# Kernel optimization log

Hardware: AMD Instinct MI355X
Metric: run time of the kernel (lower is better)

## Reference

```python
import jax, jax.numpy as jnp
import numpy as np
from jax.scipy.optimize import minimize

LAMDA = 0.01        # lamda default in MI()
N_DOMAINS = 2       # domain_label is binary (source/target)
MAXITER = 50        # BFGS iteration budget (torchmin l-bfgs analogue)


def _sq_dists(A, B):
    # squared euclidean pairwise distances == torch.cdist(A, B, p=2) ** 2
    an = jnp.sum(A * A, axis=-1)
    bn = jnp.sum(B * B, axis=-1)
    return an[:, None] + bn[None, :] - 2.0 * (A @ B.T)


def _median_sigma(sf):
    # sigma = median of nonzero squared pairwise source distances.
    # With continuous features the only zeros are the diagonal, so mask it.
    pd = jnp.maximum(_sq_dists(sf, sf), 0.0)
    pd = jnp.where(jnp.eye(pd.shape[0], dtype=bool), jnp.nan, pd)
    return jnp.nanmedian(pd)


def _build(sf, tf, y, l):
    # Gaussian kernel masked by class agreement, plus domain one-hots.
    sigma = _median_sigma(sf)
    X = jnp.concatenate([sf, tf], axis=0)              # [N, d]
    D = _sq_dists(X, X)                                 # [N, N]
    Deltay = (y[:, None] == y[None, :]).astype(X.dtype)
    K_W = jnp.exp(-D / sigma) * Deltay                  # [N, N]
    onehot = jax.nn.one_hot(l[:, 0], N_DOMAINS, dtype=X.dtype)  # [N, 2]
    KD = K_W * (onehot @ onehot.T)                      # K_W * Deltal
    w = jnp.sum(onehot, axis=0) / X.shape[0]            # domain counts / N
    return K_W, KD, onehot, w


def _div(theta, K_W, KD, onehot, w):
    # mean((K_W*Deltal) @ theta) - mean(exp((theta*K_W) @ Deltal - 1))
    # Deltal = onehot @ onehot.T (rank-2), so the second NxN @ NxN matmul
    # collapses to A = K_W @ (theta[:,None]*onehot) with column weights w.
    term1 = jnp.mean(KD @ theta)
    A = K_W @ (theta[:, None] * onehot)                 # [N, 2]
    term2 = jnp.mean(jnp.exp(A - 1.0) @ w)
    return term1 - term2


def _solve_theta(K_W, KD, onehot, w):
    N = K_W.shape[0]
    obj = lambda th: -_div(th, K_W, KD, onehot, w) + LAMDA * (th @ th)
    res = minimize(obj, jnp.zeros((N,), K_W.dtype), method="BFGS",
                   options={"maxiter": MAXITER})
    return res.x


def setup_inputs() -> dict:
    key = jax.random.key(0)
    k1, k2, k3, k4 = jax.random.split(key, 4)
    B, d, n_class = 2048, 256, 31
    source_features = jax.random.normal(k1, (B, d), dtype=jnp.float32)
    target_features = jax.random.normal(k2, (B, d), dtype=jnp.float32)
    y = jax.random.randint(k3, (2 * B,), 0, n_class, dtype=jnp.int32)
    l = jax.random.randint(k4, (2 * B, 1), 0, N_DOMAINS, dtype=jnp.int32)
    return {"source_features": source_features, "target_features": target_features,
            "y": y, "l": l}


def reference(source_features, target_features, y, l):
    K_W, KD, onehot, w = _build(source_features, target_features, y, l)
    theta_hat = _solve_theta(K_W, KD, onehot, w)
    return _div(theta_hat, K_W, KD, onehot, w)
```

## Files before the change

### kernel.cpp

```cpp
#include <hip/hip_runtime.h>
#include <math.h>

#define N_TOT   4096
#define N_SRC   2048
#define DIMF    256
#define NCLASS  31
#define LAMBDA  0.01f

#define K_TRI1  1048063LL
#define K_TRI2  1048064LL

#define WS_ACC    0
#define WS_HIST0  64
#define WS_HISTA  16448
#define WS_HISTB  32832
#define WS_H2A    49216
#define WS_H2B    50240
#define WS_STATE  51264
#define WS_TICK   51520
#define WS_META   52288
#define WS_SCAL   52800
#define ZERO_BYTES 53248
#define WS_PERM   53248
#define WS_XN     69632
#define WS_DS     1048576
#define WS_KBLK   17825792

#define MAXW 224
#define MAXM 112
#define WPAD 116

__device__ __forceinline__ float bf2f(unsigned short h) {
  return __uint_as_float(((unsigned)h) << 16);
}

__device__ __forceinline__ float wredF(float v) {
#pragma unroll
  for (int o = 1; o < 64; o <<= 1) v += __shfl_xor(v, o, 64);
  return v;
}

__device__ __forceinline__ double blockReduceSum(double v, double* red) {
#pragma unroll
  for (int o = 32; o > 0; o >>= 1) v += __shfl_down(v, o, 64);
  int w = threadIdx.x >> 6, lane = threadIdx.x & 63;
  __syncthreads();
  if (lane == 0) red[w] = v;
  __syncthreads();
  return red[0] + red[1] + red[2] + red[3];
}

__device__ __forceinline__ void blockReduceSumMax(double s, double mx, double* red,
                                                  double& os, double& om) {
#pragma unroll
  for (int o = 32; o > 0; o >>= 1) {
    s += __shfl_down(s, o, 64);
    double u = __shfl_down(mx, o, 64);
    mx = fmax(mx, u);
  }
  int w = threadIdx.x >> 6, lane = threadIdx.x & 63;
  __syncthreads();
  if (lane == 0) { red[w] = s; red[4 + w] = mx; }
  __syncthreads();
  os = red[0] + red[1] + red[2] + red[3];
  om = fmax(fmax(red[4], red[5]), fmax(red[6], red[7]));
}

__device__ void scan_find(const unsigned* hist, int nbins, long long k, unsigned* shOut, int tid) {
  __shared__ long long tsum[256];
  int per = nbins / 256;
  long long s = 0;
  for (int q = 0; q < per; q++) s += hist[tid * per + q];
  tsum[tid] = s;
  __syncthreads();
  long long acc = s;
  for (int off = 1; off < 256; off <<= 1) {
    long long add = (tid >= off) ? tsum[tid - off] : 0;
    __syncthreads();
    acc += add;
    tsum[tid] = acc;
    __syncthreads();
  }
  long long run = acc - s;
  for (int q = 0; q < per; q++) {
    unsigned c = hist[tid * per + q];
    if (k >= run && k < run + (long long)c) { shOut[0] = (unsigned)(tid * per + q); shOut[1] = (unsigned)(k - run); }
    run += c;
  }
  __syncthreads();
}

__global__ __launch_bounds__(256) void xn_kernel(const float* __restrict__ sf,
                                                 const float* __restrict__ tf,
                                                 float* __restrict__ xn,
                                                 uint4* __restrict__ wsz,
                                                 const int* __restrict__ y,
                                                 const int* __restrict__ l,
                                                 int* __restrict__ perm,
                                                 int* __restrict__ meta,
                                                 float* __restrict__ scal) {
  __shared__ unsigned cl[64];
  __shared__ unsigned bs2[64];
  __shared__ unsigned cur[64];
  const int tid = threadIdx.x;
  if (blockIdx.x == 0) {
    uint4 z; z.x = 0; z.y = 0; z.z = 0; z.w = 0;
    for (int q = tid; q < ZERO_BYTES / 16; q += 256) wsz[q] = z;
    if (tid < 64) cl[tid] = 0;
    __syncthreads();
    for (int i = tid; i < N_TOT; i += 256) atomicAdd(&cl[y[i] * 2 + l[i]], 1u);
    __syncthreads();
    if (tid == 0) {
      unsigned run = 0;
      for (int b2 = 0; b2 < 62; b2++) { bs2[b2] = run; run += cl[b2]; }
      unsigned run2 = 0, cnt0 = 0;
      for (int c = 0; c < NCLASS; c++) {
        int n = (int)(cl[2 * c] + cl[2 * c + 1]);
        meta[c] = n; meta[32 + c] = (int)cl[2 * c]; meta[64 + c] = (int)bs2[2 * c];
        meta[96 + c] = (int)run2; run2 += (unsigned)(n * n);
        cnt0 += cl[2 * c];
      }
      scal[1] = (float)((double)cnt0 / (4096.0 * 4096.0));
      scal[2] = (float)((double)(N_TOT - cnt0) / (4096.0 * 4096.0));
    }
    __syncthreads();
    if (tid < 64) cur[tid] = bs2[tid];
    __syncthreads();
    for (int i = tid; i < N_TOT; i += 256) {
      int b2 = y[i] * 2 + l[i];
      unsigned pos = atomicAdd(&cur[b2], 1u);
      perm[pos] = i;
    }
  }
  int wid = tid >> 6, lane = tid & 63;
  int row = blockIdx.x * 4 + wid;
  const float* src = (row < N_SRC) ? (sf + (size_t)row * DIMF) : (tf + (size_t)(row - N_SRC) * DIMF);
  float4 v = ((const float4*)src)[lane];
  float s = v.x * v.x + v.y * v.y + v.z * v.z + v.w * v.w;
#pragma unroll
  for (int o = 32; o > 0; o >>= 1) s += __shfl_down(s, o, 64);
  if (lane == 0) xn[row] = s;
}

__global__ __launch_bounds__(256) void dist_k(const float* __restrict__ sf,
                                              const float* __restrict__ xn,
                                              float* __restrict__ Ds,
                                              unsigned* __restrict__ h) {
  __shared__ float As[16][68];
  __shared__ float Bs[16][68];
  __shared__ unsigned lh[2][4096];
  const int tx = threadIdx.x, ty = threadIdx.y;
  const int tid = ty * 16 + tx;
  const int par = tid & 1;
  for (int q = tid; q < 8192; q += 256) lh[q >> 12][q & 4095] = 0;
  int b = blockIdx.x;
  int by = (int)((sqrtf(8.f * (float)b + 1.f) - 1.f) * 0.5f);
  while ((by + 1) * (by + 2) / 2 <= b) ++by;
  while (by * (by + 1) / 2 > b) --by;
  int bx = b - by * (by + 1) / 2;
  const int R = by * 64, C = bx * 64;
  const int si = tid >> 2, sq = tid & 3;
  float4 va = ((const float4*)(sf + (size_t)(R + si) * 256 + 0))[sq];
  float4 vb = ((const float4*)(sf + (size_t)(C + si) * 256 + 0))[sq];
  float acc[4][4] = {};
  for (int kc = 0; kc < 256; kc += 16) {
    As[sq * 4 + 0][si] = va.x; As[sq * 4 + 1][si] = va.y; As[sq * 4 + 2][si] = va.z; As[sq * 4 + 3][si] = va.w;
    Bs[sq * 4 + 0][si] = vb.x; Bs[sq * 4 + 1][si] = vb.y; Bs[sq * 4 + 2][si] = vb.z; Bs[sq * 4 + 3][si] = vb.w;
    __syncthreads();
    if (kc + 16 < 256) {
      va = ((const float4*)(sf + (size_t)(R + si) * 256 + kc + 16))[sq];
      vb = ((const float4*)(sf + (size_t)(C + si) * 256 + kc + 16))[sq];
    }
#pragma unroll
    for (int k = 0; k < 16; k++) {
      float4 a = *(const float4*)&As[k][ty * 4];
      float4 b2 = *(const float4*)&Bs[k][tx * 4];
      acc[0][0] += a.x * b2.x; acc[0][1] += a.x * b2.y; acc[0][2] += a.x * b2.z; acc[0][3] += a.x * b2.w;
      acc[1][0] += a.y * b2.x; acc[1][1] += a.y * b2.y; acc[1][2] += a.y * b2.z; acc[1][3] += a.y * b2.w;
      acc[2][0] += a.z * b2.x; acc[2][1] += a.z * b2.y; acc[2][2] += a.z * b2.z; acc[2][3] += a.z * b2.w;
      acc[3][0] += a.w * b2.x; acc[3][1] += a.w * b2.y; acc[3][2] += a.w * b2.z; acc[3][3] += a.w * b2.w;
    }
    __syncthreads();
  }
  int jbase = C + tx * 4;
  float xnj0 = xn[jbase + 0], xnj1 = xn[jbase + 1], xnj2 = xn[jbase + 2], xnj3 = xn[jbase + 3];
#pragma unroll
  for (int r = 0; r < 4; r++) {
    int i = R + ty * 4 + r;
    float xni = xn[i];
    float v[4];
    v[0] = fmaxf(xni + xnj0 - 2.f * acc[r][0], 0.f);
    v[1] = fmaxf(xni + xnj1 - 2.f * acc[r][1], 0.f);
    v[2] = fmaxf(xni + xnj2 - 2.f * acc[r][2], 0.f);
    v[3] = fmaxf(xni + xnj3 - 2.f * acc[r][3], 0.f);
    if (jbase + 3 < i) {
      float4 o; o.x = v[0]; o.y = v[1]; o.z = v[2]; o.w = v[3];
      ((float4*)&Ds[(size_t)i * 2048 + jbase])[0] = o;
      atomicAdd(&lh[par][__float_as_uint(v[0]) >> 20], 1u);
      atomicAdd(&lh[par][__float_as_uint(v[1]) >> 20], 1u);
      atomicAdd(&lh[par][__float_as_uint(v[2]) >> 20], 1u);
      atomicAdd(&lh[par][__float_as_uint(v[3]) >> 20], 1u);
    } else {
#pragma unroll
      for (int k = 0; k < 4; k++) {
        if (jbase + k < i) {
          Ds[(size_t)i * 2048 + jbase + k] = v[k];
          atomicAdd(&lh[par][__float_as_uint(v[k]) >> 20], 1u);
        }
      }
    }
  }
  __syncthreads();
  for (int q = tid; q < 4096; q += 256) {
    unsigned v = lh[0][q] + lh[1][q];
    if (v) atomicAdd(&h[q], v);
  }
}

__global__ __launch_bounds__(256) void scan0_k(const unsigned* __restrict__ h, unsigned* __restrict__ st) {
  __shared__ unsigned r0[2];
  __shared__ unsigned r1[2];
  scan_find(h, 4096, K_TRI1, r0, threadIdx.x);
  scan_find(h, 4096, K_TRI2, r1, threadIdx.x);
  if (threadIdx.x == 0) { st[0] = r0[0]; st[1] = r0[1]; st[2] = r1[0]; st[3] = r1[1]; }
}

__global__ __launch_bounds__(256) void hist1_k(const float* __restrict__ Ds, const unsigned* __restrict__ st,
                                               unsigned* __restrict__ hA, unsigned* __restrict__ hB) {
  __shared__ unsigned lA[4096];
  __shared__ unsigned lB[4096];
  for (int i = threadIdx.x; i < 4096; i += 256) { lA[i] = 0; lB[i] = 0; }
  __syncthreads();
  unsigned s0 = st[0], s1 = st[2];
  int gw = (blockIdx.x * 256 + threadIdx.x) >> 6;
  int lane = threadIdx.x & 63;
  const float* row = Ds + (size_t)gw * 2048;
  for (int j = lane; j < gw; j += 64) {
    unsigned u = __float_as_uint(row[j]);
    unsigned hi = u >> 20, mid = (u >> 8) & 0xFFFu;
    if (hi == s0) atomicAdd(&lA[mid], 1u);
    if (hi == s1) atomicAdd(&lB[mid], 1u);
  }
  __syncthreads();
  for (int i = threadIdx.x; i < 4096; i += 256) {
    if (lA[i]) atomicAdd(&hA[i], lA[i]);
    if (lB[i]) atomicAdd(&hB[i], lB[i]);
  }
}

__global__ __launch_bounds__(256) void scan1_k(const unsigned* __restrict__ hA, const unsigned* __restrict__ hB,
                                               unsigned* __restrict__ st) {
  __shared__ unsigned r0[2];
  __shared__ unsigned r1[2];
  long long kA = (long long)st[1];
  long long kB = (long long)st[3];
  scan_find(hA, 4096, kA, r0, threadIdx.x);
  scan_find(hB, 4096, kB, r1, threadIdx.x);
  if (threadIdx.x == 0) { st[4] = r0[0]; st[5] = r0[1]; st[6] = r1[0]; st[7] = r1[1]; }
}

__global__ __launch_bounds__(256) void hist2_k(const float* __restrict__ Ds, const unsigned* __restrict__ st,
                                               unsigned* __restrict__ hA, unsigned* __restrict__ hB) {
  __shared__ unsigned lA[256];
  __shared__ unsigned lB[256];
  lA[threadIdx.x] = 0; lB[threadIdx.x] = 0;
  __syncthreads();
  unsigned p0 = (st[0] << 12) | st[4];
  unsigned p1 = (st[2] << 12) | st[6];
  int gw = (blockIdx.x * 256 + threadIdx.x) >> 6;
  int lane = threadIdx.x & 63;
  const float* row = Ds + (size_t)gw * 2048;
  for (int j = lane; j < gw; j += 64) {
    unsigned u = __float_as_uint(row[j]);
    unsigned pre = u >> 8;
    if (pre == p0) atomicAdd(&lA[u & 0xFFu], 1u);
    if (pre == p1) atomicAdd(&lB[u & 0xFFu], 1u);
  }
  __syncthreads();
  if (lA[threadIdx.x]) atomicAdd(&hA[threadIdx.x], lA[threadIdx.x]);
  if (lB[threadIdx.x]) atomicAdd(&hB[threadIdx.x], lB[threadIdx.x]);
}

__global__ __launch_bounds__(256) void scan2b_k(const unsigned* __restrict__ hA, const unsigned* __restrict__ hB,
                                                const unsigned* __restrict__ st, float* __restrict__ scal) {
  int tid = threadIdx.x;
  __shared__ unsigned r0[2];
  __shared__ unsigned r1[2];
  scan_find(hA, 256, (long long)st[5], r0, tid);
  scan_find(hB, 256, (long long)st[7], r1, tid);
  if (tid == 0) {
    unsigned v1 = (st[0] << 20) | (st[4] << 8) | r0[0];
    unsigned v2 = (st[2] << 20) | (st[6] << 8) | r1[0];
    scal[0] = 0.5f * (__uint_as_float(v1) + __uint_as_float(v2));
  }
}

__global__ __launch_bounds__(256) void build_k(const float* __restrict__ sf, const float* __restrict__ tf,
                                               const float* __restrict__ xn, const int* __restrict__ perm,
                                               const int* __restrict__ meta, const float* __restrict__ scal,
                                               float* __restrict__ gK) {
  const int c = blockIdx.z;
  const int n = meta[c];
  const int cs = meta[64 + c];
  const int bo = meta[96 + c];
  const int T = (n + 15) >> 4;
  int b = blockIdx.x;
  if (b >= T * (T + 1) / 2) return;
  int by = (int)((sqrtf(8.f * (float)b + 1.f) - 1.f) * 0.5f);
  while ((by + 1) * (by + 2) / 2 <= b) ++by;
  while (by * (by + 1) / 2 > b) --by;
  int bx = b - by * (by + 1) / 2;
  const int i0 = by * 16, j0 = bx * 16;
  const int tx = threadIdx.x, ty = threadIdx.y;
  __shared__ float As[16][260];
  __shared__ float Bs[16][260];
  __shared__ float ot[16][17];
  __shared__ int ra[16];
  __shared__ int rb[16];
  int tid = ty * 16 + tx;
  if (tid < 16) { int il = i0 + tid; ra[tid] = (il < n) ? perm[cs + il] : -1; }
  else if (tid < 32) { int jl = j0 + tid - 16; rb[tid - 16] = (jl < n) ? perm[cs + jl] : -1; }
  __syncthreads();
  for (int e = tid; e < 1024; e += 256) {
    int r = e >> 6, q = e & 63;
    int g = ra[r];
    if (g >= 0) {
      const float* src = (g < N_SRC) ? (sf + (size_t)g * DIMF) : (tf + (size_t)(g - N_SRC) * DIMF);
      ((float4*)&As[r][q * 4])[0] = ((const float4*)src)[q];
    }
    int g2 = rb[r];
    if (g2 >= 0) {
      const float* src = (g2 < N_SRC) ? (sf + (size_t)g2 * DIMF) : (tf + (size_t)(g2 - N_SRC) * DIMF);
      ((float4*)&Bs[r][q * 4])[0] = ((const float4*)src)[q];
    }
  }
  __syncthreads();
  int il = i0 + ty, jl = j0 + tx;
  float val = 0.f;
  if (il < n && jl < n) {
    float dot = 0.f;
    const float4* a4 = (const float4*)&As[ty][0];
    const float4* b4 = (const float4*)&Bs[tx][0];
#pragma unroll 16
    for (int q = 0; q < 64; q++) {
      float4 a = a4[q], b2 = b4[q];
      dot += a.x * b2.x + a.y * b2.y + a.z * b2.z + a.w * b2.w;
    }
    int gi = ra[ty], gj = rb[tx];
    float d = xn[gi] + xn[gj] - 2.f * dot;
    val = expf(-d / scal[0]);
    gK[(size_t)bo + (size_t)il * n + jl] = val;
  }
  ot[ty][tx] = val;
  __syncthreads();
  if (by != bx) {
    int il2 = j0 + ty, jl2 = i0 + tx;
    if (il2 < n && jl2 < n) gK[(size_t)bo + (size_t)il2 * n + jl2] = ot[tx][ty];
  }
}

__global__ __launch_bounds__(256) void solver_k(const float* __restrict__ gK, const int* __restrict__ meta,
                                                const float* __restrict__ scal, double* __restrict__ acc,
                                                unsigned* __restrict__ tick, float* __restrict__ out) {
  const int c = blockIdx.x >> 1, d = blockIdx.x & 1;
  const int n = meta[c];
  const int m0 = meta[32 + c];
  const int m = d ? (n - m0) : m0;
  const int c0 = d ? m0 : 0;
  const int bo = meta[96 + c];
  const float gamma = scal[1 + d];
  const int tid = threadIdx.x;
  const int wv = tid >> 6, lane = tid & 63;

  __shared__ unsigned short Wl[MAXW * WPAD];
  __shared__ float pS[4 * MAXM];
  __shared__ float pD[4 * MAXM];
  __shared__ float Av[MAXW];
  __shared__ float Sv[MAXW];
  __shared__ float Uv[MAXW];
  __shared__ float bc[MAXM];
  __shared__ float gv[MAXM];
  __shared__ float dgv[MAXM];
  __shared__ alignas(16) float th[128];
  __shared__ alignas(16) float pv[128];
  __shared__ alignas(16) float xv[128];
  __shared__ double red[16];
  __shared__ double gds[2];
  __shared__ float alf_s[2];
  __shared__ int cgst[2];

  const float* K = gK + bo;
  const int st = n;
  const int mp2 = (m + 1) & ~1;
  const int mp4 = (m + 3) & ~3;
  const int iw0 = (n * wv) >> 2, iw1 = (n * (wv + 1)) >> 2;
  const int rq = tid >> 2, ql = tid & 3;

  for (int i = rq; i < n; i += 64) {
    const float* Kr = K + (size_t)i * st + c0;
    unsigned short* Wr = Wl + i * WPAD;
    for (int j = ql; j < m; j += 4) {
      unsigned u = __float_as_uint(Kr[j]);
      u += 0x7fffu + ((u >> 16) & 1u);
      Wr[j] = (unsigned short)(u >> 16);
    }
    if (ql == 0) for (int j = m; j < mp4; j++) Wr[j] = 0;
  }
  for (int j = rq; j < m; j += 64) {
    const float* Kr = K + (size_t)(c0 + j) * st + c0;
    float s = 0.f;
    for (int r = ql; r < m; r += 4) s += Kr[r];
    s += __shfl_xor(s, 1, 64);
    s += __shfl_xor(s, 2, 64);
    if (ql == 0) bc[j] = s * (1.0f / 4096.0f);
  }
  __syncthreads();
  for (int j = tid; j < 128; j += 256) { th[j] = 0.f; pv[j] = 0.f; xv[j] = 0.f; }
  __syncthreads();

  float av_r = 0.f;

  for (int it = 0; it < 25; it++) {
    double o = 0.0;
    if (it == 0) {
      const float s0c = gamma * expf(-1.f);
      av_r = 0.f;
      for (int i = tid; i < n; i += 256) { Sv[i] = s0c; o += (double)s0c; }
    } else {
      for (int i = tid; i < n; i += 256) {
        const unsigned short* Wr = Wl + i * WPAD;
        float a = 0.f;
#pragma unroll 4
        for (int j = 0; j < mp4; j += 4) {
          unsigned long long u = *(const unsigned long long*)(Wr + j);
          float4 t4 = *(const float4*)(th + j);
          unsigned lo = (unsigned)u, hi = (unsigned)(u >> 32);
          a += __uint_as_float(lo << 16) * t4.x
             + __uint_as_float(lo & 0xffff0000u) * t4.y
             + __uint_as_float(hi << 16) * t4.z
             + __uint_as_float(hi & 0xffff0000u) * t4.w;
        }
        av_r = a;
        float si = gamma * expf(fminf(a - 1.f, 30.f));
        Sv[i] = si; o += (double)si;
      }
      for (int j = tid; j < m; j += 256) {
        float t_ = th[j];
        o += (double)(-bc[j] * t_ + LAMBDA * t_ * t_);
      }
    }
    __syncthreads();
    if (it == 0) {
      for (int j = lane; j < m; j += 64) {
        const unsigned short* Wc = Wl + j;
        float s_ = 0.f, ds_ = 0.f;
        int i = iw0;
        for (; i + 3 < iw1; i += 4) {
          float w0 = bf2f(Wc[(i + 0) * WPAD]), w1 = bf2f(Wc[(i + 1) * WPAD]);
          float w2 = bf2f(Wc[(i + 2) * WPAD]), w3 = bf2f(Wc[(i + 3) * WPAD]);
          float a0 = w0 * Sv[i], a1 = w1 * Sv[i + 1], a2 = w2 * Sv[i + 2], a3 = w3 * Sv[i + 3];
          s_ += a0 + a1 + a2 + a3;
          ds_ += a0 * w0 + a1 * w1 + a2 * w2 + a3 * w3;
        }
        for (; i < iw1; i++) { float w = bf2f(Wc[i * WPAD]); float a = w * Sv[i]; s_ += a; ds_ += a * w; }
        pS[wv * MAXM + j] = s_; pD[wv * MAXM + j] = ds_;
      }
    } else {
      for (int j = lane; j < m; j += 64) {
        const unsigned short* Wc = Wl + j;
        float s_ = 0.f;
        int i = iw0;
        for (; i + 3 < iw1; i += 4)
          s_ += bf2f(Wc[(i+0)*WPAD]) * Sv[i]   + bf2f(Wc[(i+1)*WPAD]) * Sv[i+1]
              + bf2f(Wc[(i+2)*WPAD]) * Sv[i+2] + bf2f(Wc[(i+3)*WPAD]) * Sv[i+3];
        for (; i < iw1; i++) s_ += bf2f(Wc[i * WPAD]) * Sv[i];
        pS[wv * MAXM + j] = s_;
      }
    }
    __syncthreads();
    double gm = 0.0;
    for (int j = tid; j < m; j += 256) {
      float s_ = pS[j] + pS[MAXM + j] + pS[2 * MAXM + j] + pS[3 * MAXM + j];
      if (it == 0) {
        float ds_ = pD[j] + pD[MAXM + j] + pD[2 * MAXM + j] + pD[3 * MAXM + j];
        dgv[j] = ds_ + 2.f * LAMBDA;
      }
      float g = s_ - bc[j] + 2.f * LAMBDA * th[j];
      gv[j] = g;
      double ag = fabs((double)g); if (ag > gm) gm = ag;
    }
    double obj, gmax;
    blockReduceSumMax(o, gm, red, obj, gmax);
    if (gmax < 1e-5) break;

    const float tolf = (it == 0) ? 1e-2f : ((it == 1) ? 1e-3f : 1e-4f);
    float p0 = 0.f, p1 = 0.f, r0 = 0.f, r1 = 0.f, z0 = 0.f, z1 = 0.f, x0 = 0.f, x1 = 0.f;
    float dg0 = 1.f, dg1 = 1.f, rzf = 0.f, rz0f = 0.f;
    float bq = 0.f, wp = 0.f;
    double gtpacc = 0.0;
    const int j0 = lane, j1 = lane + 64;
    if (wv == 0) {
      if (j0 < m) { dg0 = dgv[j0]; r0 = -gv[j0]; z0 = r0 / dg0; }
      if (j1 < m) { dg1 = dgv[j1]; r1 = -gv[j1]; z1 = r1 / dg1; }
      p0 = z0; p1 = z1;
      rzf = wredF(r0 * z0 + r1 * z1);
      rz0f = rzf;
      pv[j0] = p0; pv[j1] = p1;
      if (lane == 0) { cgst[0] = (rzf > 0.f) ? 0 : 1; cgst[1] = 0; }
    }
    __syncthreads();
    bool brk = false;
    for (int cg = 0; cg < 12; cg++) {
      if (cgst[1]) bq += alf_s[0] * wp;
      if (cgst[0]) { brk = true; break; }
      for (int i = tid; i < n; i += 256) {
        const unsigned short* Wr = Wl + i * WPAD;
        float a = 0.f;
#pragma unroll 4
        for (int j = 0; j < mp4; j += 4) {
          unsigned long long u = *(const unsigned long long*)(Wr + j);
          float4 t4 = *(const float4*)(pv + j);
          unsigned lo = (unsigned)u, hi = (unsigned)(u >> 32);
          a += __uint_as_float(lo << 16) * t4.x
             + __uint_as_float(lo & 0xffff0000u) * t4.y
             + __uint_as_float(hi << 16) * t4.z
             + __uint_as_float(hi & 0xffff0000u) * t4.w;
        }
        wp = a;
        Uv[i] = a * Sv[i];
      }
      __syncthreads();
      for (int j = lane; j < m; j += 64) {
        const unsigned short* Wc = Wl + j;
        float q = 0.f;
        int i = iw0;
        for (; i + 3 < iw1; i += 4)
          q += bf2f(Wc[(i+0)*WPAD]) * Uv[i]   + bf2f(Wc[(i+1)*WPAD]) * Uv[i+1]
             + bf2f(Wc[(i+2)*WPAD]) * Uv[i+2] + bf2f(Wc[(i+3)*WPAD]) * Uv[i+3];
        for (; i < iw1; i++) q += bf2f(Wc[i * WPAD]) * Uv[i];
        pS[wv * MAXM + j] = q;
      }
      __syncthreads();
      if (wv == 0) {
        float q0 = 0.f, q1 = 0.f;
        if (j0 < m) q0 = pS[j0] + pS[MAXM + j0] + pS[2*MAXM + j0] + pS[3*MAXM + j0] + 2.f * LAMBDA * p0;
        if (j1 < m) q1 = pS[j1] + pS[MAXM + j1] + pS[2*MAXM + j1] + pS[3*MAXM + j1] + 2.f * LAMBDA * p1;
        float pq = wredF(p0 * q0 + p1 * q1);
        int stop = 0;
        if (!(pq > 0.f)) {
          stop = 1;
          if (lane == 0) cgst[1] = 0;
        } else {
          float alpha = rzf / pq;
          gtpacc += (double)alpha * (double)rzf;
          x0 += alpha * p0; x1 += alpha * p1;
          r0 -= alpha * q0; r1 -= alpha * q1;
          z0 = r0 / dg0;    z1 = r1 / dg1;
          if (lane == 0) { alf_s[0] = alpha; cgst[1] = 1; }
          float rzn = wredF(r0 * z0 + r1 * z1);
          if (rzn < tolf * rz0f || cg == 11) stop = 1;
          else {
            float beta = rzn / rzf;
            p0 = z0 + beta * p0; p1 = z1 + beta * p1;
            pv[j0] = p0; pv[j1] = p1;
            rzf = rzn;
          }
        }
        if (lane == 0) cgst[0] = stop;
      }
      __syncthreads();
    }
    if (!brk && cgst[1]) bq += alf_s[0] * wp;
    if (wv == 0) {
      xv[j0] = x0; xv[j1] = x1;
      if (lane == 0) gds[0] = -gtpacc;
    }
    __syncthreads();
    double gtp = gds[0];
    if (!(gtp < 0.0)) break;

    float t = 1.f;
    if (-gtp >= 1e-4) {
      for (int ls = 0; ls < 10; ls++) {
        double ol = 0.0;
        if (tid < n) ol += (double)(gamma * expf(fminf(av_r + t * bq - 1.f, 30.f)));
        for (int j = tid; j < m; j += 256) {
          float tj = th[j] + t * xv[j];
          ol += (double)(-bc[j] * tj + LAMBDA * tj * tj);
        }
        double ot2 = blockReduceSum(ol, red);
        if (ot2 <= obj + 1e-4 * (double)t * gtp) break;
        t *= 0.5f;
      }
    }
    for (int j = tid; j < mp2; j += 256) th[j] += t * xv[j];
    __syncthreads();
  }

  __syncthreads();
  for (int i = rq; i < n; i += 64) {
    const float* Kr = K + (size_t)i * st + c0;
    float a = 0.f;
#pragma unroll 4
    for (int j = ql; j < m; j += 4) a += th[j] * Kr[j];
    a += __shfl_xor(a, 1, 64);
    a += __shfl_xor(a, 2, 64);
    if (ql == 0) Av[i] = a;
  }
  __syncthreads();
  double t1l = 0.0, t2l = 0.0;
  for (int i = tid; i < n; i += 256) t2l += (double)(gamma * expf(fminf(Av[i] - 1.f, 30.f)));
  for (int j = tid; j < m; j += 256) t1l += (double)(bc[j] * th[j]);
  double t1 = blockReduceSum(t1l, red);
  double t2 = blockReduceSum(t2l, red);
  if (tid == 0) {
    atomicAdd(&acc[0], t1);
    atomicAdd(&acc[1], t2);
    __threadfence();
    unsigned old = __hip_atomic_fetch_add(&tick[0], 1u, __ATOMIC_ACQ_REL, __HIP_MEMORY_SCOPE_AGENT);
    if (old == 61u) {
      double a0 = __hip_atomic_load(&acc[0], __ATOMIC_RELAXED, __HIP_MEMORY_SCOPE_AGENT);
      double a1 = __hip_atomic_load(&acc[1], __ATOMIC_RELAXED, __HIP_MEMORY_SCOPE_AGENT);
      out[0] = (float)(a0 - a1);
    }
  }
}

extern "C" void kernel_launch(void* const* d_in, const int* in_sizes, int n_in,
                              void* d_out, int out_size, void* d_ws, size_t ws_size,
                              hipStream_t stream) {
  const float* sf = (const float*)d_in[0];
  const float* tf = (const float*)d_in[1];
  const int* y = (const int*)d_in[2];
  const int* l = (const int*)d_in[3];
  char* ws = (char*)d_ws;

  double*   acc    = (double*)(ws + WS_ACC);
  unsigned* hist0  = (unsigned*)(ws + WS_HIST0);
  unsigned* histA  = (unsigned*)(ws + WS_HISTA);
  unsigned* histB  = (unsigned*)(ws + WS_HISTB);
  unsigned* h2A    = (unsigned*)(ws + WS_H2A);
  unsigned* h2B    = (unsigned*)(ws + WS_H2B);
  unsigned* state  = (unsigned*)(ws + WS_STATE);
  unsigned* tick   = (unsigned*)(ws + WS_TICK);
  int*      meta   = (int*)(ws + WS_META);
  float*    scal   = (float*)(ws + WS_SCAL);
  int*      perm   = (int*)(ws + WS_PERM);
  float*    xnp    = (float*)(ws + WS_XN);
  float*    Ds     = (float*)(ws + WS_DS);
  float*    gK     = (float*)(ws + WS_KBLK);

  hipLaunchKernelGGL(xn_kernel, dim3(1024), dim3(256), 0, stream, sf, tf, xnp, (uint4*)ws, y, l, perm, meta, scal);
  hipLaunchKernelGGL(dist_k, dim3(528), dim3(16, 16), 0, stream, sf, xnp, Ds, hist0);
  hipLaunchKernelGGL(scan0_k, dim3(1), dim3(256), 0, stream, hist0, state);
  hipLaunchKernelGGL(hist1_k, dim3(512), dim3(256), 0, stream, Ds, state, histA, histB);
  hipLaunchKernelGGL(scan1_k, dim3(1), dim3(256), 0, stream, histA, histB, state);
  hipLaunchKernelGGL(hist2_k, dim3(512), dim3(256), 0, stream, Ds, state, h2A, h2B);
  hipLaunchKernelGGL(scan2b_k, dim3(1), dim3(256), 0, stream, h2A, h2B, state, scal);
  hipLaunchKernelGGL(build_k, dim3(105, 1, NCLASS), dim3(16, 16), 0, stream, sf, tf, xnp, perm, meta, scal, gK);
  hipLaunchKernelGGL(solver_k, dim3(62), dim3(256), 0, stream, gK, meta, scal, acc, tick, (float*)d_out);
}
```

Before: 205.3 us.

## Fold radix-select scans into histogram kernels and unroll solver dot loops

The single-block scan0/scan1 kernels are removed. Block 0 of hist1_k and hist2_k now does the scan and publishes the selected bin and rank through a flagged 64-bit atomic, while the other blocks spin-poll for it. This cuts two kernel launches and their serialization gaps. scan_find now uses a wavefront shuffle prefix instead of a barrier-heavy shared-memory scan. The solver's bf16 mat-vec loops use two independent accumulators to expose more ILP. The spin-wait relies on block 0 being scheduled and on the state flags being zeroed before each run (WS_STATE lies inside the zeroed region). Changing the accumulation order slightly alters floating-point rounding.

```diff
diff --git a/kernel.cpp b/kernel.cpp
--- a/kernel.cpp
+++ b/kernel.cpp
@@ -30,8 +30,24 @@
 #define MAXM 112
 #define WPAD 116
 
+#define PK_BIN(v)  ((unsigned)((v) & 0x1FFFULL))
+#define PK_RANK(v) ((long long)(((v) >> 13) & 0x3FFFFFFULL))
+
 __device__ __forceinline__ float bf2f(unsigned short h) {
   return __uint_as_float(((unsigned)h) << 16);
+}
+
+__device__ __forceinline__ void pub64(unsigned long long* p, unsigned bin, unsigned rank) {
+  unsigned long long v = (1ULL << 63) | ((unsigned long long)rank << 13) | (unsigned long long)bin;
+  __hip_atomic_store(p, v, __ATOMIC_RELAXED, __HIP_MEMORY_SCOPE_AGENT);
+}
+__device__ __forceinline__ unsigned long long poll64(const unsigned long long* p) {
+  unsigned long long v = __hip_atomic_load(p, __ATOMIC_RELAXED, __HIP_MEMORY_SCOPE_AGENT);
+  while (!(v >> 63)) {
+    __builtin_amdgcn_s_sleep(8);
+    v = __hip_atomic_load(p, __ATOMIC_RELAXED, __HIP_MEMORY_SCOPE_AGENT);
+  }
+  return v;
 }
 
 __device__ __forceinline__ float wredF(float v) {
@@ -67,21 +83,22 @@
 }
 
 __device__ void scan_find(const unsigned* hist, int nbins, long long k, unsigned* shOut, int tid) {
-  __shared__ long long tsum[256];
-  int per = nbins / 256;
+  __shared__ long long wsum[4];
+  const int per = nbins >> 8;
+  const int lane = tid & 63, wv = tid >> 6;
   long long s = 0;
   for (int q = 0; q < per; q++) s += hist[tid * per + q];
-  tsum[tid] = s;
-  __syncthreads();
-  long long acc = s;
-  for (int off = 1; off < 256; off <<= 1) {
-    long long add = (tid >= off) ? tsum[tid - off] : 0;
-    __syncthreads();
-    acc += add;
-    tsum[tid] = acc;
-    __syncthreads();
-  }
-  long long run = acc - s;
+  long long inc = s;
+#pragma unroll
+  for (int o = 1; o < 64; o <<= 1) {
+    long long u = __shfl_up(inc, o, 64);
+    if (lane >= o) inc += u;
+  }
+  if (lane == 63) wsum[wv] = inc;
+  __syncthreads();
+  long long base = 0;
+  for (int w = 0; w < wv; w++) base += wsum[w];
+  long long run = base + inc - s;
   for (int q = 0; q < per; q++) {
     unsigned c = hist[tid * per + q];
     if (k >= run && k < run + (long long)c) { shOut[0] = (unsigned)(tid * per + q); shOut[1] = (unsigned)(k - run); }
@@ -217,23 +234,37 @@
   }
 }
 
-__global__ __launch_bounds__(256) void scan0_k(const unsigned* __restrict__ h, unsigned* __restrict__ st) {
-  __shared__ unsigned r0[2];
-  __shared__ unsigned r1[2];
-  scan_find(h, 4096, K_TRI1, r0, threadIdx.x);
-  scan_find(h, 4096, K_TRI2, r1, threadIdx.x);
-  if (threadIdx.x == 0) { st[0] = r0[0]; st[1] = r0[1]; st[2] = r1[0]; st[3] = r1[1]; }
-}
-
-__global__ __launch_bounds__(256) void hist1_k(const float* __restrict__ Ds, const unsigned* __restrict__ st,
+__global__ __launch_bounds__(256) void hist1_k(const float* __restrict__ Ds,
+                                               const unsigned* __restrict__ h0,
+                                               unsigned long long* __restrict__ stp,
                                                unsigned* __restrict__ hA, unsigned* __restrict__ hB) {
   __shared__ unsigned lA[4096];
   __shared__ unsigned lB[4096];
-  for (int i = threadIdx.x; i < 4096; i += 256) { lA[i] = 0; lB[i] = 0; }
-  __syncthreads();
-  unsigned s0 = st[0], s1 = st[2];
-  int gw = (blockIdx.x * 256 + threadIdx.x) >> 6;
-  int lane = threadIdx.x & 63;
+  __shared__ unsigned sb[2];
+  const int tid = threadIdx.x;
+  for (int i = tid; i < 4096; i += 256) { lA[i] = 0; lB[i] = 0; }
+  if (blockIdx.x == 0) {
+    __shared__ unsigned r0[2];
+    __shared__ unsigned r1[2];
+    scan_find(h0, 4096, K_TRI1, r0, tid);
+    scan_find(h0, 4096, K_TRI2, r1, tid);
+    if (tid == 0) {
+      pub64(&stp[0], r0[0], r0[1]);
+      pub64(&stp[1], r1[0], r1[1]);
+      sb[0] = r0[0]; sb[1] = r1[0];
+    }
+    __syncthreads();
+  } else {
+    if (tid == 0) {
+      unsigned long long v0 = poll64(&stp[0]);
+      unsigned long long v1 = poll64(&stp[1]);
+      sb[0] = PK_BIN(v0); sb[1] = PK_BIN(v1);
+    }
+    __syncthreads();
+  }
+  unsigned s0 = sb[0], s1 = sb[1];
+  int gw = (blockIdx.x * 256 + tid) >> 6;
+  int lane = tid & 63;
   const float* row = Ds + (size_t)gw * 2048;
   for (int j = lane; j < gw; j += 64) {
     unsigned u = __float_as_uint(row[j]);
@@ -242,33 +273,49 @@
     if (hi == s1) atomicAdd(&lB[mid], 1u);
   }
   __syncthreads();
-  for (int i = threadIdx.x; i < 4096; i += 256) {
+  for (int i = tid; i < 4096; i += 256) {
     if (lA[i]) atomicAdd(&hA[i], lA[i]);
     if (lB[i]) atomicAdd(&hB[i], lB[i]);
   }
 }
 
-__global__ __launch_bounds__(256) void scan1_k(const unsigned* __restrict__ hA, const unsigned* __restrict__ hB,
-                                               unsigned* __restrict__ st) {
-  __shared__ unsigned r0[2];
-  __shared__ unsigned r1[2];
-  long long kA = (long long)st[1];
-  long long kB = (long long)st[3];
-  scan_find(hA, 4096, kA, r0, threadIdx.x);
-  scan_find(hB, 4096, kB, r1, threadIdx.x);
-  if (threadIdx.x == 0) { st[4] = r0[0]; st[5] = r0[1]; st[6] = r1[0]; st[7] = r1[1]; }
-}
-
-__global__ __launch_bounds__(256) void hist2_k(const float* __restrict__ Ds, const unsigned* __restrict__ st,
-                                               unsigned* __restrict__ hA, unsigned* __restrict__ hB) {
+__global__ __launch_bounds__(256) void hist2_k(const float* __restrict__ Ds,
+                                               const unsigned* __restrict__ hA,
+                                               const unsigned* __restrict__ hB,
+                                               unsigned long long* __restrict__ stp,
+                                               unsigned* __restrict__ h2A, unsigned* __restrict__ h2B) {
   __shared__ unsigned lA[256];
   __shared__ unsigned lB[256];
-  lA[threadIdx.x] = 0; lB[threadIdx.x] = 0;
-  __syncthreads();
-  unsigned p0 = (st[0] << 12) | st[4];
-  unsigned p1 = (st[2] << 12) | st[6];
-  int gw = (blockIdx.x * 256 + threadIdx.x) >> 6;
-  int lane = threadIdx.x & 63;
+  __shared__ unsigned sp[2];
+  const int tid = threadIdx.x;
+  lA[tid] = 0; lB[tid] = 0;
+  unsigned long long v0 = __hip_atomic_load(&stp[0], __ATOMIC_RELAXED, __HIP_MEMORY_SCOPE_AGENT);
+  unsigned long long v1 = __hip_atomic_load(&stp[1], __ATOMIC_RELAXED, __HIP_MEMORY_SCOPE_AGENT);
+  unsigned st0 = PK_BIN(v0), st2 = PK_BIN(v1);
+  if (blockIdx.x == 0) {
+    __shared__ unsigned r0[2];
+    __shared__ unsigned r1[2];
+    scan_find(hA, 4096, PK_RANK(v0), r0, tid);
+    scan_find(hB, 4096, PK_RANK(v1), r1, tid);
+    if (tid == 0) {
+      pub64(&stp[2], r0[0], r0[1]);
+      pub64(&stp[3], r1[0], r1[1]);
+      sp[0] = (st0 << 12) | r0[0];
+      sp[1] = (st2 << 12) | r1[0];
+    }
+    __syncthreads();
+  } else {
+    if (tid == 0) {
+      unsigned long long w2 = poll64(&stp[2]);
+      unsigned long long w3 = poll64(&stp[3]);
+      sp[0] = (st0 << 12) | PK_BIN(w2);
+      sp[1] = (st2 << 12) | PK_BIN(w3);
+    }
+    __syncthreads();
+  }
+  unsigned p0 = sp[0], p1 = sp[1];
+  int gw = (blockIdx.x * 256 + tid) >> 6;
+  int lane = tid & 63;
   const float* row = Ds + (size_t)gw * 2048;
   for (int j = lane; j < gw; j += 64) {
     unsigned u = __float_as_uint(row[j]);
@@ -277,21 +324,25 @@
     if (pre == p1) atomicAdd(&lB[u & 0xFFu], 1u);
   }
   __syncthreads();
-  if (lA[threadIdx.x]) atomicAdd(&hA[threadIdx.x], lA[threadIdx.x]);
-  if (lB[threadIdx.x]) atomicAdd(&hB[threadIdx.x], lB[threadIdx.x]);
+  if (lA[tid]) atomicAdd(&h2A[tid], lA[tid]);
+  if (lB[tid]) atomicAdd(&h2B[tid], lB[tid]);
 }
 
 __global__ __launch_bounds__(256) void scan2b_k(const unsigned* __restrict__ hA, const unsigned* __restrict__ hB,
-                                                const unsigned* __restrict__ st, float* __restrict__ scal) {
+                                                const unsigned long long* __restrict__ stp,
+                                                float* __restrict__ scal) {
   int tid = threadIdx.x;
   __shared__ unsigned r0[2];
   __shared__ unsigned r1[2];
-  scan_find(hA, 256, (long long)st[5], r0, tid);
-  scan_find(hB, 256, (long long)st[7], r1, tid);
+  unsigned long long v0 = stp[0], v1 = stp[1], v2 = stp[2], v3 = stp[3];
+  unsigned st0 = PK_BIN(v0), st2 = PK_BIN(v1);
+  unsigned st4 = PK_BIN(v2), st6 = PK_BIN(v3);
+  scan_find(hA, 256, PK_RANK(v2), r0, tid);
+  scan_find(hB, 256, PK_RANK(v3), r1, tid);
   if (tid == 0) {
-    unsigned v1 = (st[0] << 20) | (st[4] << 8) | r0[0];
-    unsigned v2 = (st[2] << 20) | (st[6] << 8) | r1[0];
-    scal[0] = 0.5f * (__uint_as_float(v1) + __uint_as_float(v2));
+    unsigned b1 = (st0 << 20) | (st4 << 8) | r0[0];
+    unsigned b2 = (st2 << 20) | (st6 << 8) | r1[0];
+    scal[0] = 0.5f * (__uint_as_float(b1) + __uint_as_float(b2));
   }
 }
 
@@ -429,17 +480,28 @@
     } else {
       for (int i = tid; i < n; i += 256) {
         const unsigned short* Wr = Wl + i * WPAD;
-        float a = 0.f;
-#pragma unroll 4
-        for (int j = 0; j < mp4; j += 4) {
+        float aa = 0.f, ab = 0.f;
+        int j = 0;
+        for (; j + 7 < mp4; j += 8) {
+          unsigned long long u1 = *(const unsigned long long*)(Wr + j);
+          float4 t1 = *(const float4*)(th + j);
+          unsigned lo1 = (unsigned)u1, hi1 = (unsigned)(u1 >> 32);
+          aa += __uint_as_float(lo1 << 16) * t1.x + __uint_as_float(lo1 & 0xffff0000u) * t1.y
+              + __uint_as_float(hi1 << 16) * t1.z + __uint_as_float(hi1 & 0xffff0000u) * t1.w;
+          unsigned long long u2 = *(const unsigned long long*)(Wr + j + 4);
+          float4 t2 = *(const float4*)(th + j + 4);
+          unsigned lo2 = (unsigned)u2, hi2 = (unsigned)(u2 >> 32);
+          ab += __uint_as_float(lo2 << 16) * t2.x + __uint_as_float(lo2 & 0xffff0000u) * t2.y
+              + __uint_as_float(hi2 << 16) * t2.z + __uint_as_float(hi2 & 0xffff0000u) * t2.w;
+        }
+        for (; j < mp4; j += 4) {
           unsigned long long u = *(const unsigned long long*)(Wr + j);
           float4 t4 = *(const float4*)(th + j);
           unsigned lo = (unsigned)u, hi = (unsigned)(u >> 32);
-          a += __uint_as_float(lo << 16) * t4.x
-             + __uint_as_float(lo & 0xffff0000u) * t4.y
-             + __uint_as_float(hi << 16) * t4.z
-             + __uint_as_float(hi & 0xffff0000u) * t4.w;
-        }
+          aa += __uint_as_float(lo << 16) * t4.x + __uint_as_float(lo & 0xffff0000u) * t4.y
+              + __uint_as_float(hi << 16) * t4.z + __uint_as_float(hi & 0xffff0000u) * t4.w;
+        }
+        float a = aa + ab;
         av_r = a;
         float si = gamma * expf(fminf(a - 1.f, 30.f));
         Sv[i] = si; o += (double)si;
@@ -468,13 +530,16 @@
     } else {
       for (int j = lane; j < m; j += 64) {
         const unsigned short* Wc = Wl + j;
-        float s_ = 0.f;
+        float sa = 0.f, sb = 0.f;
         int i = iw0;
-        for (; i + 3 < iw1; i += 4)
-          s_ += bf2f(Wc[(i+0)*WPAD]) * Sv[i]   + bf2f(Wc[(i+1)*WPAD]) * Sv[i+1]
+        for (; i + 7 < iw1; i += 8) {
+          sa += bf2f(Wc[(i+0)*WPAD]) * Sv[i]   + bf2f(Wc[(i+1)*WPAD]) * Sv[i+1]
               + bf2f(Wc[(i+2)*WPAD]) * Sv[i+2] + bf2f(Wc[(i+3)*WPAD]) * Sv[i+3];
-        for (; i < iw1; i++) s_ += bf2f(Wc[i * WPAD]) * Sv[i];
-        pS[wv * MAXM + j] = s_;
+          sb += bf2f(Wc[(i+4)*WPAD]) * Sv[i+4] + bf2f(Wc[(i+5)*WPAD]) * Sv[i+5]
+              + bf2f(Wc[(i+6)*WPAD]) * Sv[i+6] + bf2f(Wc[(i+7)*WPAD]) * Sv[i+7];
+        }
+        for (; i < iw1; i++) sa += bf2f(Wc[i * WPAD]) * Sv[i];
+        pS[wv * MAXM + j] = sa + sb;
       }
     }
     __syncthreads();
@@ -515,30 +580,44 @@
       if (cgst[0]) { brk = true; break; }
       for (int i = tid; i < n; i += 256) {
         const unsigned short* Wr = Wl + i * WPAD;
-        float a = 0.f;
-#pragma unroll 4
-        for (int j = 0; j < mp4; j += 4) {
+        float aa = 0.f, ab = 0.f;
+        int j = 0;
+        for (; j + 7 < mp4; j += 8) {
+          unsigned long long u1 = *(const unsigned long long*)(Wr + j);
+          float4 t1 = *(const float4*)(pv + j);
+          unsigned lo1 = (unsigned)u1, hi1 = (unsigned)(u1 >> 32);
+          aa += __uint_as_float(lo1 << 16) * t1.x + __uint_as_float(lo1 & 0xffff0000u) * t1.y
+              + __uint_as_float(hi1 << 16) * t1.z + __uint_as_float(hi1 & 0xffff0000u) * t1.w;
+          unsigned long long u2 = *(const unsigned long long*)(Wr + j + 4);
+          float4 t2 = *(const float4*)(pv + j + 4);
+          unsigned lo2 = (unsigned)u2, hi2 = (unsigned)(u2 >> 32);
+          ab += __uint_as_float(lo2 << 16) * t2.x + __uint_as_float(lo2 & 0xffff0000u) * t2.y
+              + __uint_as_float(hi2 << 16) * t2.z + __uint_as_float(hi2 & 0xffff0000u) * t2.w;
+        }
+        for (; j < mp4; j += 4) {
           unsigned long long u = *(const unsigned long long*)(Wr + j);
           float4 t4 = *(const float4*)(pv + j);
           unsigned lo = (unsigned)u, hi = (unsigned)(u >> 32);
-          a += __uint_as_float(lo << 16) * t4.x
-             + __uint_as_float(lo & 0xffff0000u) * t4.y
-             + __uint_as_float(hi << 16) * t4.z
-             + __uint_as_float(hi & 0xffff0000u) * t4.w;
-        }
+          aa += __uint_as_float(lo << 16) * t4.x + __uint_as_float(lo & 0xffff0000u) * t4.y
+              + __uint_as_float(hi << 16) * t4.z + __uint_as_float(hi & 0xffff0000u) * t4.w;
+        }
+        float a = aa + ab;
         wp = a;
         Uv[i] = a * Sv[i];
       }
       __syncthreads();
       for (int j = lane; j < m; j += 64) {
         const unsigned short* Wc = Wl + j;
-        float q = 0.f;
+        float qa = 0.f, qb = 0.f;
         int i = iw0;
-        for (; i + 3 < iw1; i += 4)
-          q += bf2f(Wc[(i+0)*WPAD]) * Uv[i]   + bf2f(Wc[(i+1)*WPAD]) * Uv[i+1]
-             + bf2f(Wc[(i+2)*WPAD]) * Uv[i+2] + bf2f(Wc[(i+3)*WPAD]) * Uv[i+3];
-        for (; i < iw1; i++) q += bf2f(Wc[i * WPAD]) * Uv[i];
-        pS[wv * MAXM + j] = q;
+        for (; i + 7 < iw1; i += 8) {
+          qa += bf2f(Wc[(i+0)*WPAD]) * Uv[i]   + bf2f(Wc[(i+1)*WPAD]) * Uv[i+1]
+              + bf2f(Wc[(i+2)*WPAD]) * Uv[i+2] + bf2f(Wc[(i+3)*WPAD]) * Uv[i+3];
+          qb += bf2f(Wc[(i+4)*WPAD]) * Uv[i+4] + bf2f(Wc[(i+5)*WPAD]) * Uv[i+5]
+              + bf2f(Wc[(i+6)*WPAD]) * Uv[i+6] + bf2f(Wc[(i+7)*WPAD]) * Uv[i+7];
+        }
+        for (; i < iw1; i++) qa += bf2f(Wc[i * WPAD]) * Uv[i];
+        pS[wv * MAXM + j] = qa + qb;
       }
       __syncthreads();
       if (wv == 0) {
@@ -641,7 +720,7 @@
   unsigned* histB  = (unsigned*)(ws + WS_HISTB);
   unsigned* h2A    = (unsigned*)(ws + WS_H2A);
   unsigned* h2B    = (unsigned*)(ws + WS_H2B);
-  unsigned* state  = (unsigned*)(ws + WS_STATE);
+  unsigned long long* stp = (unsigned long long*)(ws + WS_STATE);
   unsigned* tick   = (unsigned*)(ws + WS_TICK);
   int*      meta   = (int*)(ws + WS_META);
   float*    scal   = (float*)(ws + WS_SCAL);
@@ -652,11 +731,9 @@
 
   hipLaunchKernelGGL(xn_kernel, dim3(1024), dim3(256), 0, stream, sf, tf, xnp, (uint4*)ws, y, l, perm, meta, scal);
   hipLaunchKernelGGL(dist_k, dim3(528), dim3(16, 16), 0, stream, sf, xnp, Ds, hist0);
-  hipLaunchKernelGGL(scan0_k, dim3(1), dim3(256), 0, stream, hist0, state);
-  hipLaunchKernelGGL(hist1_k, dim3(512), dim3(256), 0, stream, Ds, state, histA, histB);
-  hipLaunchKernelGGL(scan1_k, dim3(1), dim3(256), 0, stream, histA, histB, state);
-  hipLaunchKernelGGL(hist2_k, dim3(512), dim3(256), 0, stream, Ds, state, h2A, h2B);
-  hipLaunchKernelGGL(scan2b_k, dim3(1), dim3(256), 0, stream, h2A, h2B, state, scal);
+  hipLaunchKernelGGL(hist1_k, dim3(512), dim3(256), 0, stream, Ds, hist0, stp, histA, histB);
+  hipLaunchKernelGGL(hist2_k, dim3(512), dim3(256), 0, stream, Ds, histA, histB, stp, h2A, h2B);
+  hipLaunchKernelGGL(scan2b_k, dim3(1), dim3(256), 0, stream, h2A, h2B, stp, scal);
   hipLaunchKernelGGL(build_k, dim3(105, 1, NCLASS), dim3(16, 16), 0, stream, sf, tf, xnp, perm, meta, scal, gK);
   hipLaunchKernelGGL(solver_k, dim3(62), dim3(256), 0, stream, gK, meta, scal, acc, tick, (float*)d_out);
 }
```

Result: slower. 209.9 us (+2.2%).
